# Kernel tuning notes

Measured on AMD Instinct MI355X. Metric: run time of the kernel, lower is better.

Reference implementation:

```python
import jax, jax.numpy as jnp
import numpy as np

HEADS = 4
DIM_HEAD = 32


def setup_inputs() -> dict:
    key = jax.random.key(0)
    k0, k1, k2, k3 = jax.random.split(key, 4)
    b, C, H, W = 32, 128, 64, 64
    hidden = HEADS * DIM_HEAD
    x = jax.random.normal(k0, (b, C, H, W), dtype=jnp.float32)
    g = jnp.ones((C,), dtype=jnp.float32)                      # RMSNorm gain
    w_qkv = jax.random.normal(k1, (3 * hidden, C), dtype=jnp.float32) * 0.05
    mem_kv = jax.random.normal(k2, (2, HEADS, DIM_HEAD, 4), dtype=jnp.float32)
    w_out = jax.random.normal(k3, (C, hidden), dtype=jnp.float32) * 0.05
    b_out = jnp.zeros((C,), dtype=jnp.float32)
    return {"x": x, "g": g, "w_qkv": w_qkv, "mem_kv": mem_kv,
            "w_out": w_out, "b_out": b_out}


def reference(x, g, w_qkv, mem_kv, w_out, b_out):
    b, C, H, W = x.shape
    heads = mem_kv.shape[1]
    dh = mem_kv.shape[2]
    hidden = heads * dh
    scale = dh ** -0.5

    # RMSNorm variant: F.normalize along channel dim * g * sqrt(C)
    norm = jnp.maximum(jnp.sqrt(jnp.sum(x * x, axis=1, keepdims=True)), 1e-12)
    xn = x / norm * g[None, :, None, None] * (C ** 0.5)

    # 1x1 conv qkv projection (no bias)
    qkv = jnp.einsum('bchw,oc->bohw', xn, w_qkv)  # [b, 3*hidden, H, W]
    q, k, v = jnp.split(qkv, 3, axis=1)
    n = H * W
    q = q.reshape(b, heads, dh, n)
    k = k.reshape(b, heads, dh, n)
    v = v.reshape(b, heads, dh, n)

    # prepend memory kv slots along the token dim
    mk = jnp.broadcast_to(mem_kv[0][None], (b, heads, dh, mem_kv.shape[3]))
    mv = jnp.broadcast_to(mem_kv[1][None], (b, heads, dh, mem_kv.shape[3]))
    k = jnp.concatenate([mk, k], axis=-1)
    v = jnp.concatenate([mv, v], axis=-1)

    q = jax.nn.softmax(q, axis=-2) * scale   # softmax over feature dim d
    k = jax.nn.softmax(k, axis=-1)           # softmax over token dim n

    context = jnp.einsum('bhdn,bhen->bhde', k, v)   # [b,h,d,e]
    out = jnp.einsum('bhde,bhdn->bhen', context, q)  # [b,h,e,n]
    out = out.reshape(b, hidden, H, W)

    # 1x1 conv output projection (with bias)
    return jnp.einsum('bchw,oc->bohw', out, w_out) + b_out[None, :, None, None]
```

## Files before the change

kernel.cpp:

```cpp
#include <hip/hip_runtime.h>
#include <hip/hip_bf16.h>

typedef __attribute__((ext_vector_type(8))) short short8;
typedef __attribute__((ext_vector_type(4))) short bf16x4;
typedef __attribute__((ext_vector_type(4))) float f32x4;


__device__ __forceinline__ unsigned short f2bf(float f) {
  unsigned u = __float_as_uint(f);
  u += 0x7fff + ((u >> 16) & 1);
  return (unsigned short)(u >> 16);
}
__device__ __forceinline__ float bf2f(unsigned short s) {
  return __uint_as_float(((unsigned)s) << 16);
}

__global__ void k0_init(const float* __restrict__ wqkv, const float* __restrict__ g,
                        float* __restrict__ ws) {
  int tid = blockIdx.x * blockDim.x + threadIdx.x;
  int stride = gridDim.x * blockDim.x;
  unsigned short* Wf = (unsigned short*)(ws + 2424832);
  for (int i = tid; i < 49152; i += stride) {
    int o = i >> 7, c = i & 127;
    int f = (o >> 4) * 4 + (c >> 5);
    int lane = (o & 15) + (((c >> 3) & 3) << 4);
    Wf[f * 512 + lane * 8 + (c & 7)] = f2bf(wqkv[o * 128 + c]);
  }
  float* gs = ws + 2449408;
  if (tid < 128) gs[tid] = g[tid] * 11.313708498984761f;
}

__global__ __launch_bounds__(256, 2) void k1_qkv(
    const float* __restrict__ x, const unsigned short* __restrict__ Wf,
    const float* __restrict__ gs, unsigned short* __restrict__ Sp,
    unsigned short* __restrict__ Zp, unsigned short* __restrict__ qbf) {
  __shared__ __align__(16) unsigned short xnf[16 * 512];
  __shared__ __align__(16) unsigned short kbuf[128 * 64];
  __shared__ __align__(16) unsigned short vbuf[128 * 64];
  __shared__ float ssred[256];
  const int b = blockIdx.x >> 4, grp = blockIdx.x & 15;
  const int tid = threadIdx.x;
  const int p = tid & 63, w = tid >> 6;
  const int chunk = __builtin_amdgcn_readfirstlane(w);
  const int l = p, quad = l >> 4, l16 = l & 15;

  short8 ones;
#pragma unroll
  for (int j = 0; j < 8; j++) ones[j] = (short)0x3F80;

  f32x4 accS[2][2] = {};
  f32x4 accZ[2] = {};

  const float* xbase = x + (size_t)b * 524288;
  float xr[32];
  {
    const float* xb = xbase + grp * 256 + p;
#pragma unroll
    for (int i = 0; i < 32; i++) xr[i] = xb[(size_t)(chunk * 32 + i) * 4096];
  }

#pragma unroll 1
  for (int t = 0; t < 4; t++) {
    const int tile = grp * 4 + t;
    float ss = 0.f;
#pragma unroll
    for (int i = 0; i < 32; i++) ss += xr[i] * xr[i];
    ssred[w * 64 + p] = ss;
    __syncthreads();
    float tot = ssred[p] + ssred[64 + p] + ssred[128 + p] + ssred[192 + p];
    float inv = 1.0f / fmaxf(sqrtf(tot), 1e-12f);
#pragma unroll
    for (int q8 = 0; q8 < 4; q8++) {
      short8 v8;
#pragma unroll
      for (int j = 0; j < 8; j++) {
        int i = q8 * 8 + j;
        v8[j] = (short)f2bf(xr[i] * gs[chunk * 32 + i] * inv);
      }
      *(short8*)&xnf[(chunk * 4 + (p >> 4)) * 512 + ((p & 15) + q8 * 16) * 8] = v8;
    }
    __syncthreads();

    if (t < 3) {
      const float* xb = xbase + (tile + 1) * 64 + p;
#pragma unroll
      for (int i = 0; i < 32; i++) xr[i] = xb[(size_t)(chunk * 32 + i) * 4096];
    }

    const short8* Wfv = (const short8*)Wf;
#pragma unroll
    for (int s = 0; s < 3; s++) {
      f32x4 acc[2][4] = {};
#pragma unroll
      for (int k0 = 0; k0 < 4; k0++) {
        short8 bfr[4];
#pragma unroll
        for (int n0 = 0; n0 < 4; n0++)
          bfr[n0] = *(const short8*)&xnf[(k0 * 4 + n0) * 512 + l * 8];
#pragma unroll
        for (int off = 0; off < 2; off++) {
          short8 afr = Wfv[((s * 8 + chunk * 2 + off) * 4 + k0) * 64 + l];
#pragma unroll
          for (int n0 = 0; n0 < 4; n0++)
            acc[off][n0] = __builtin_amdgcn_mfma_f32_16x16x32_bf16(afr, bfr[n0], acc[off][n0], 0, 0, 0);
        }
      }
      if (s == 0) {
#pragma unroll
        for (int n0 = 0; n0 < 4; n0++) {
          float m = -1e30f;
#pragma unroll
          for (int off = 0; off < 2; off++)
#pragma unroll
            for (int r = 0; r < 4; r++) m = fmaxf(m, acc[off][n0][r]);
          m = fmaxf(m, __shfl_xor(m, 16, 64));
          m = fmaxf(m, __shfl_xor(m, 32, 64));
          float e[2][4]; float sum = 0.f;
#pragma unroll
          for (int off = 0; off < 2; off++)
#pragma unroll
            for (int r = 0; r < 4; r++) {
              e[off][r] = __expf(acc[off][n0][r] - m);
              sum += e[off][r];
            }
          sum += __shfl_xor(sum, 16, 64);
          sum += __shfl_xor(sum, 32, 64);
          float rs = 0.17677669529663687f / sum;
          int qbase = ((b * 64 + tile) * 16 + chunk * 4 + n0) * 512;
#pragma unroll
          for (int off = 0; off < 2; off++) {
            int lane2 = l16 + ((off * 2 + (quad >> 1)) << 4);
            bf16x4 qv;
#pragma unroll
            for (int r = 0; r < 4; r++) qv[r] = (short)f2bf(e[off][r] * rs);
            *(bf16x4*)&qbf[qbase + lane2 * 8 + (quad & 1) * 4] = qv;
          }
        }
      } else if (s == 1) {
#pragma unroll
        for (int off = 0; off < 2; off++)
#pragma unroll
          for (int n0 = 0; n0 < 4; n0++)
#pragma unroll
            for (int r = 0; r < 4; r++) {
              int row = off * 16 + quad * 4 + r;
              int px = n0 * 16 + l16;
              kbuf[(chunk * 32 + row) * 64 + (px ^ ((row & 7) << 3))] = f2bf(__expf(acc[off][n0][r]));
            }
      } else {
#pragma unroll
        for (int off = 0; off < 2; off++)
#pragma unroll
          for (int n0 = 0; n0 < 4; n0++)
#pragma unroll
            for (int r = 0; r < 4; r++) {
              int row = off * 16 + quad * 4 + r;
              int px = n0 * 16 + l16;
              vbuf[(chunk * 32 + row) * 64 + (px ^ ((row & 7) << 3))] = f2bf(acc[off][n0][r]);
            }
      }
    }

    const unsigned short* kb = kbuf + chunk * 2048;
    const unsigned short* vb = vbuf + chunk * 2048;
#pragma unroll
    for (int kk = 0; kk < 2; kk++) {
      int cofs = (kk * 32 + quad * 8) ^ ((l16 & 7) << 3);
      short8 ak[2], av[2];
#pragma unroll
      for (int mm = 0; mm < 2; mm++) {
        ak[mm] = *(const short8*)&kb[(mm * 16 + l16) * 64 + cofs];
        av[mm] = *(const short8*)&vb[(mm * 16 + l16) * 64 + cofs];
      }
#pragma unroll
      for (int mm = 0; mm < 2; mm++) {
#pragma unroll
        for (int nn = 0; nn < 2; nn++)
          accS[mm][nn] = __builtin_amdgcn_mfma_f32_16x16x32_bf16(ak[mm], av[nn], accS[mm][nn], 0, 0, 0);
        accZ[mm] = __builtin_amdgcn_mfma_f32_16x16x32_bf16(ak[mm], ones, accZ[mm], 0, 0, 0);
      }
    }
  }

  unsigned short* Spb = Sp + (size_t)(b * 16 + grp) * 4096 + chunk * 1024;
#pragma unroll
  for (int mm = 0; mm < 2; mm++)
#pragma unroll
    for (int nn = 0; nn < 2; nn++) {
      bf16x4 sv;
#pragma unroll
      for (int r = 0; r < 4; r++) sv[r] = (short)f2bf(accS[mm][nn][r]);
      *(bf16x4*)&Spb[(mm * 2 + nn) * 256 + l * 4] = sv;
    }
  if (l16 == 0) {
#pragma unroll
    for (int mm = 0; mm < 2; mm++) {
      bf16x4 zv;
#pragma unroll
      for (int r = 0; r < 4; r++) zv[r] = (short)f2bf(accZ[mm][r]);
      *(bf16x4*)&Zp[(b * 16 + grp) * 128 + chunk * 32 + mm * 16 + quad * 4] = zv;
    }
  }
}

__global__ __launch_bounds__(256) void k2_ctx(
    const unsigned short* __restrict__ Sp, const unsigned short* __restrict__ Zp,
    const float* __restrict__ memkv, const float* __restrict__ wout,
    unsigned short* __restrict__ Mtf) {
  __shared__ float wl[128 * 33];
  __shared__ float Cs[8 * 32];
  __shared__ float zsh[8];
  __shared__ float zinv_s[8];
  const int b = blockIdx.x >> 4, sl = blockIdx.x & 15, tid = threadIdx.x;
  const int hd0 = sl * 8, h = hd0 >> 5;
  for (int i = tid; i < 4096; i += 256) {
    int o = i >> 5, e = i & 31;
    wl[o * 33 + e] = wout[o * 128 + h * 32 + e];
  }
  {
    int hdi = tid >> 5, g = tid & 31;
    float zp = (g < 16) ? bf2f(Zp[(b * 16 + g) * 128 + hd0 + hdi]) : 0.f;
#pragma unroll
    for (int s2 = 1; s2 < 32; s2 <<= 1) zp += __shfl_xor(zp, s2, 32);
    if (g == 0) zsh[hdi] = zp;
  }
  __syncthreads();
  if (tid < 8) {
    int hd = hd0 + tid;
    float zm = 0.f;
#pragma unroll
    for (int j = 0; j < 4; j++) zm += __expf(memkv[hd * 4 + j]);
    zinv_s[tid] = 1.0f / (zsh[tid] + zm);
  }
  __syncthreads();
  {
    int hdi = tid >> 5, e = tid & 31;
    int hd = hd0 + hdi, d = hd & 31;
    int fofs = h * 1024 + ((d >> 4) * 2 + (e >> 4)) * 256 + ((e & 15) + ((d >> 2) & 3) * 16) * 4 + (d & 3);
    const unsigned short* Spb = Sp + (size_t)b * 65536 + fofs;
    float s = 0.f;
#pragma unroll
    for (int g = 0; g < 16; g++) s += bf2f(Spb[g * 4096]);
    float sm = 0.f;
#pragma unroll
    for (int j = 0; j < 4; j++)
      sm += __expf(memkv[hd * 4 + j]) * memkv[512 + (h * 32 + e) * 4 + j];
    Cs[hdi * 32 + e] = (s + sm) * zinv_s[hdi];
  }
  __syncthreads();
  for (int i = tid; i < 1024; i += 256) {
    int o = i & 127, hdi = i >> 7;
    float a = 0.f;
#pragma unroll
    for (int e = 0; e < 32; e++) a += wl[o * 33 + e] * Cs[hdi * 32 + e];
    int hd = hd0 + hdi;
    int f = (o >> 4) * 4 + h;
    int lane = (o & 15) + (((hd >> 3) & 3) << 4);
    Mtf[(size_t)b * 16384 + f * 512 + lane * 8 + (hd & 7)] = f2bf(a);
  }
}

__global__ __launch_bounds__(256) void k3_out(
    const unsigned short* __restrict__ qbf, const unsigned short* __restrict__ Mtf,
    const float* __restrict__ bout, float* __restrict__ out) {
  const int b = blockIdx.x >> 6, tile = blockIdx.x & 63;
  const int tid = threadIdx.x;
  const int l = tid & 63, quad = l >> 4, l16 = l & 15;
  const int chunk = __builtin_amdgcn_readfirstlane(tid >> 6);
  const short8* Mv = (const short8*)Mtf;
  const short8* qv = (const short8*)qbf + (size_t)(b * 64 + tile) * 1024;
  short8 afr[2][4];
#pragma unroll
  for (int mm = 0; mm < 2; mm++)
#pragma unroll
    for (int k0 = 0; k0 < 4; k0++)
      afr[mm][k0] = Mv[((size_t)b * 32 + (chunk * 2 + mm) * 4 + k0) * 64 + l];
  f32x4 acc[2][4] = {};
#pragma unroll
  for (int hh = 0; hh < 2; hh++) {
    short8 bfr[8];
#pragma unroll
    for (int j = 0; j < 8; j++) bfr[j] = qv[(hh * 8 + j) * 64 + l];
#pragma unroll
    for (int kk = 0; kk < 2; kk++) {
      int k0 = hh * 2 + kk;
#pragma unroll
      for (int mm = 0; mm < 2; mm++)
#pragma unroll
        for (int n0 = 0; n0 < 4; n0++)
          acc[mm][n0] = __builtin_amdgcn_mfma_f32_16x16x32_bf16(afr[mm][k0], bfr[kk * 4 + n0], acc[mm][n0], 0, 0, 0);
    }
  }
  float* ob = out + (size_t)b * 524288 + tile * 64;
#pragma unroll
  for (int mm = 0; mm < 2; mm++)
#pragma unroll
    for (int r = 0; r < 4; r++) {
      int o = chunk * 32 + mm * 16 + quad * 4 + r;
      float bv = bout[o];
#pragma unroll
      for (int n0 = 0; n0 < 4; n0++)
        ob[(size_t)o * 4096 + n0 * 16 + l16] = acc[mm][n0][r] + bv;
    }
}

extern "C" void kernel_launch(void* const* d_in, const int* in_sizes, int n_in,
                              void* d_out, int out_size, void* d_ws, size_t ws_size,
                              hipStream_t stream) {
  const float* x     = (const float*)d_in[0];
  const float* g     = (const float*)d_in[1];
  const float* wqkv  = (const float*)d_in[2];
  const float* memkv = (const float*)d_in[3];
  const float* wout  = (const float*)d_in[4];
  const float* bout  = (const float*)d_in[5];
  float* out = (float*)d_out;
  float* ws = (float*)d_ws;
  unsigned short* Sp  = (unsigned short*)ws;
  unsigned short* Zp  = (unsigned short*)(ws + 2097152);
  unsigned short* Mtf = (unsigned short*)(ws + 2162688);
  unsigned short* Wf  = (unsigned short*)(ws + 2424832);
  float* gs  = ws + 2449408;
  unsigned short* qbf = (unsigned short*)(ws + 2449536);

  k0_init<<<128, 256, 0, stream>>>(wqkv, g, ws);
  k1_qkv<<<512, 256, 0, stream>>>(x, Wf, gs, Sp, Zp, qbf);
  k2_ctx<<<512, 256, 0, stream>>>(Sp, Zp, memkv, wout, Mtf);
  k3_out<<<2048, 256, 0, stream>>>(qbf, Mtf, bout, out);
}
```

Before: 187.5 us.

## Fuse four kernels into one persistent kernel with global atomic barriers

Merges the weight-prep, QKV/context-partial, context-reduce and output-projection kernels into a single 512-block kernel. Grid-wide atomic spin barriers separate the phases, and the counters are zeroed by a memset before launch. This removes three kernel launch gaps and tail effects. In exchange it needs all 512 blocks co-resident (2 per CU via launch bounds) to avoid deadlock, and the k3 phase now runs 4 tiles per block instead of 2048 separate blocks.

```diff
diff --git a/kernel.cpp b/kernel.cpp
--- a/kernel.cpp
+++ b/kernel.cpp
@@ -15,293 +15,315 @@
   return __uint_as_float(((unsigned)s) << 16);
 }
 
-__global__ void k0_init(const float* __restrict__ wqkv, const float* __restrict__ g,
-                        float* __restrict__ ws) {
-  int tid = blockIdx.x * blockDim.x + threadIdx.x;
-  int stride = gridDim.x * blockDim.x;
-  unsigned short* Wf = (unsigned short*)(ws + 2424832);
-  for (int i = tid; i < 49152; i += stride) {
-    int o = i >> 7, c = i & 127;
-    int f = (o >> 4) * 4 + (c >> 5);
-    int lane = (o & 15) + (((c >> 3) & 3) << 4);
-    Wf[f * 512 + lane * 8 + (c & 7)] = f2bf(wqkv[o * 128 + c]);
-  }
-  float* gs = ws + 2449408;
-  if (tid < 128) gs[tid] = g[tid] * 11.313708498984761f;
-}
-
-__global__ __launch_bounds__(256, 2) void k1_qkv(
-    const float* __restrict__ x, const unsigned short* __restrict__ Wf,
-    const float* __restrict__ gs, unsigned short* __restrict__ Sp,
-    unsigned short* __restrict__ Zp, unsigned short* __restrict__ qbf) {
-  __shared__ __align__(16) unsigned short xnf[16 * 512];
-  __shared__ __align__(16) unsigned short kbuf[128 * 64];
-  __shared__ __align__(16) unsigned short vbuf[128 * 64];
-  __shared__ float ssred[256];
-  const int b = blockIdx.x >> 4, grp = blockIdx.x & 15;
+__device__ __forceinline__ void gbar(unsigned* c, unsigned nb) {
+  __threadfence();
+  __syncthreads();
+  if (threadIdx.x == 0) {
+    atomicAdd(c, 1u);
+    while (__hip_atomic_load(c, __ATOMIC_RELAXED, __HIP_MEMORY_SCOPE_AGENT) < nb)
+      __builtin_amdgcn_s_sleep(2);
+  }
+  __syncthreads();
+  __threadfence();
+}
+
+__global__ __launch_bounds__(256, 2) void fused(
+    const float* __restrict__ x, const float* __restrict__ gvec,
+    const float* __restrict__ wqkv, const float* __restrict__ memkv,
+    const float* __restrict__ wout, const float* __restrict__ bout,
+    float* __restrict__ out, float* __restrict__ ws) {
+  __shared__ __align__(16) unsigned char smem[50176];
+
+  const int bid = blockIdx.x;
+  const int b = bid >> 4, grp = bid & 15;
   const int tid = threadIdx.x;
   const int p = tid & 63, w = tid >> 6;
   const int chunk = __builtin_amdgcn_readfirstlane(w);
   const int l = p, quad = l >> 4, l16 = l & 15;
 
-  short8 ones;
-#pragma unroll
-  for (int j = 0; j < 8; j++) ones[j] = (short)0x3F80;
-
-  f32x4 accS[2][2] = {};
-  f32x4 accZ[2] = {};
-
-  const float* xbase = x + (size_t)b * 524288;
-  float xr[32];
+  unsigned short* Sp  = (unsigned short*)ws;
+  unsigned short* Zp  = (unsigned short*)(ws + 2097152);
+  unsigned*       cnt = (unsigned*)(ws + 2129920);
+  unsigned short* Mtf = (unsigned short*)(ws + 2162688);
+  unsigned short* Wf  = (unsigned short*)(ws + 2424832);
+  float* gs           = ws + 2449408;
+  unsigned short* qbf = (unsigned short*)(ws + 2449536);
+
   {
-    const float* xb = xbase + grp * 256 + p;
-#pragma unroll
-    for (int i = 0; i < 32; i++) xr[i] = xb[(size_t)(chunk * 32 + i) * 4096];
-  }
+    int gtid = bid * 256 + tid;
+    if (gtid < 49152) {
+      int o = gtid >> 7, c = gtid & 127;
+      int f = (o >> 4) * 4 + (c >> 5);
+      int lane = (o & 15) + (((c >> 3) & 3) << 4);
+      Wf[f * 512 + lane * 8 + (c & 7)] = f2bf(wqkv[o * 128 + c]);
+    }
+    if (gtid < 128) gs[gtid] = gvec[gtid] * 11.313708498984761f;
+  }
+  gbar(cnt + 0, 512);
+
+  {
+    unsigned short* xnf  = (unsigned short*)smem;
+    unsigned short* kbuf = (unsigned short*)(smem + 16384);
+    unsigned short* vbuf = (unsigned short*)(smem + 32768);
+    float* ssred         = (float*)(smem + 49152);
+
+    short8 ones;
+#pragma unroll
+    for (int j = 0; j < 8; j++) ones[j] = (short)0x3F80;
+
+    f32x4 accS[2][2] = {};
+    f32x4 accZ[2] = {};
+
+    const float* xbase = x + (size_t)b * 524288;
+    float xr[32];
+    {
+      const float* xb = xbase + grp * 256 + p;
+#pragma unroll
+      for (int i = 0; i < 32; i++) xr[i] = xb[(size_t)(chunk * 32 + i) * 4096];
+    }
 
 #pragma unroll 1
-  for (int t = 0; t < 4; t++) {
-    const int tile = grp * 4 + t;
-    float ss = 0.f;
-#pragma unroll
-    for (int i = 0; i < 32; i++) ss += xr[i] * xr[i];
-    ssred[w * 64 + p] = ss;
+    for (int t = 0; t < 4; t++) {
+      const int tile = grp * 4 + t;
+      float ss = 0.f;
+#pragma unroll
+      for (int i = 0; i < 32; i++) ss += xr[i] * xr[i];
+      ssred[w * 64 + p] = ss;
+      __syncthreads();
+      float tot = ssred[p] + ssred[64 + p] + ssred[128 + p] + ssred[192 + p];
+      float inv = 1.0f / fmaxf(sqrtf(tot), 1e-12f);
+#pragma unroll
+      for (int q8 = 0; q8 < 4; q8++) {
+        short8 v8;
+#pragma unroll
+        for (int j = 0; j < 8; j++) {
+          int i = q8 * 8 + j;
+          v8[j] = (short)f2bf(xr[i] * gs[chunk * 32 + i] * inv);
+        }
+        *(short8*)&xnf[(chunk * 4 + (p >> 4)) * 512 + ((p & 15) + q8 * 16) * 8] = v8;
+      }
+      __syncthreads();
+
+      if (t < 3) {
+        const float* xb = xbase + (tile + 1) * 64 + p;
+#pragma unroll
+        for (int i = 0; i < 32; i++) xr[i] = xb[(size_t)(chunk * 32 + i) * 4096];
+      }
+
+      const short8* Wfv = (const short8*)Wf;
+#pragma unroll
+      for (int s = 0; s < 3; s++) {
+        f32x4 acc[2][4] = {};
+#pragma unroll
+        for (int k0 = 0; k0 < 4; k0++) {
+          short8 bfr[4];
+#pragma unroll
+          for (int n0 = 0; n0 < 4; n0++)
+            bfr[n0] = *(const short8*)&xnf[(k0 * 4 + n0) * 512 + l * 8];
+#pragma unroll
+          for (int off = 0; off < 2; off++) {
+            short8 afr = Wfv[((s * 8 + chunk * 2 + off) * 4 + k0) * 64 + l];
+#pragma unroll
+            for (int n0 = 0; n0 < 4; n0++)
+              acc[off][n0] = __builtin_amdgcn_mfma_f32_16x16x32_bf16(afr, bfr[n0], acc[off][n0], 0, 0, 0);
+          }
+        }
+        if (s == 0) {
+#pragma unroll
+          for (int n0 = 0; n0 < 4; n0++) {
+            float m = -1e30f;
+#pragma unroll
+            for (int off = 0; off < 2; off++)
+#pragma unroll
+              for (int r = 0; r < 4; r++) m = fmaxf(m, acc[off][n0][r]);
+            m = fmaxf(m, __shfl_xor(m, 16, 64));
+            m = fmaxf(m, __shfl_xor(m, 32, 64));
+            float e[2][4]; float sum = 0.f;
+#pragma unroll
+            for (int off = 0; off < 2; off++)
+#pragma unroll
+              for (int r = 0; r < 4; r++) {
+                e[off][r] = __expf(acc[off][n0][r] - m);
+                sum += e[off][r];
+              }
+            sum += __shfl_xor(sum, 16, 64);
+            sum += __shfl_xor(sum, 32, 64);
+            float rs = 0.17677669529663687f / sum;
+            int qbase = ((b * 64 + tile) * 16 + chunk * 4 + n0) * 512;
+#pragma unroll
+            for (int off = 0; off < 2; off++) {
+              int lane2 = l16 + ((off * 2 + (quad >> 1)) << 4);
+              bf16x4 qv;
+#pragma unroll
+              for (int r = 0; r < 4; r++) qv[r] = (short)f2bf(e[off][r] * rs);
+              *(bf16x4*)&qbf[qbase + lane2 * 8 + (quad & 1) * 4] = qv;
+            }
+          }
+        } else if (s == 1) {
+#pragma unroll
+          for (int off = 0; off < 2; off++)
+#pragma unroll
+            for (int n0 = 0; n0 < 4; n0++)
+#pragma unroll
+              for (int r = 0; r < 4; r++) {
+                int row = off * 16 + quad * 4 + r;
+                int px = n0 * 16 + l16;
+                kbuf[(chunk * 32 + row) * 64 + (px ^ ((row & 7) << 3))] = f2bf(__expf(acc[off][n0][r]));
+              }
+        } else {
+#pragma unroll
+          for (int off = 0; off < 2; off++)
+#pragma unroll
+            for (int n0 = 0; n0 < 4; n0++)
+#pragma unroll
+              for (int r = 0; r < 4; r++) {
+                int row = off * 16 + quad * 4 + r;
+                int px = n0 * 16 + l16;
+                vbuf[(chunk * 32 + row) * 64 + (px ^ ((row & 7) << 3))] = f2bf(acc[off][n0][r]);
+              }
+        }
+      }
+
+      const unsigned short* kb = kbuf + chunk * 2048;
+      const unsigned short* vb = vbuf + chunk * 2048;
+#pragma unroll
+      for (int kk = 0; kk < 2; kk++) {
+        int cofs = (kk * 32 + quad * 8) ^ ((l16 & 7) << 3);
+        short8 ak[2], av[2];
+#pragma unroll
+        for (int mm = 0; mm < 2; mm++) {
+          ak[mm] = *(const short8*)&kb[(mm * 16 + l16) * 64 + cofs];
+          av[mm] = *(const short8*)&vb[(mm * 16 + l16) * 64 + cofs];
+        }
+#pragma unroll
+        for (int mm = 0; mm < 2; mm++) {
+#pragma unroll
+          for (int nn = 0; nn < 2; nn++)
+            accS[mm][nn] = __builtin_amdgcn_mfma_f32_16x16x32_bf16(ak[mm], av[nn], accS[mm][nn], 0, 0, 0);
+          accZ[mm] = __builtin_amdgcn_mfma_f32_16x16x32_bf16(ak[mm], ones, accZ[mm], 0, 0, 0);
+        }
+      }
+    }
+
+    unsigned short* Spb = Sp + (size_t)(b * 16 + grp) * 4096 + chunk * 1024;
+#pragma unroll
+    for (int mm = 0; mm < 2; mm++)
+#pragma unroll
+      for (int nn = 0; nn < 2; nn++) {
+        bf16x4 sv;
+#pragma unroll
+        for (int r = 0; r < 4; r++) sv[r] = (short)f2bf(accS[mm][nn][r]);
+        *(bf16x4*)&Spb[(mm * 2 + nn) * 256 + l * 4] = sv;
+      }
+    if (l16 == 0) {
+#pragma unroll
+      for (int mm = 0; mm < 2; mm++) {
+        bf16x4 zv;
+#pragma unroll
+        for (int r = 0; r < 4; r++) zv[r] = (short)f2bf(accZ[mm][r]);
+        *(bf16x4*)&Zp[(b * 16 + grp) * 128 + chunk * 32 + mm * 16 + quad * 4] = zv;
+      }
+    }
+  }
+  gbar(cnt + 1, 512);
+
+  {
+    float* wl     = (float*)smem;
+    float* Cs     = (float*)(smem + 16896);
+    float* zsh    = (float*)(smem + 17920);
+    float* zinv_s = (float*)(smem + 17952);
+    const int sl = grp;
+    const int hd0 = sl * 8, h = hd0 >> 5;
+    for (int i = tid; i < 4096; i += 256) {
+      int o = i >> 5, e = i & 31;
+      wl[o * 33 + e] = wout[o * 128 + h * 32 + e];
+    }
+    {
+      int hdi = tid >> 5, g = tid & 31;
+      float zp = (g < 16) ? bf2f(Zp[(b * 16 + g) * 128 + hd0 + hdi]) : 0.f;
+#pragma unroll
+      for (int s2 = 1; s2 < 32; s2 <<= 1) zp += __shfl_xor(zp, s2, 32);
+      if (g == 0) zsh[hdi] = zp;
+    }
     __syncthreads();
-    float tot = ssred[p] + ssred[64 + p] + ssred[128 + p] + ssred[192 + p];
-    float inv = 1.0f / fmaxf(sqrtf(tot), 1e-12f);
-#pragma unroll
-    for (int q8 = 0; q8 < 4; q8++) {
-      short8 v8;
-#pragma unroll
-      for (int j = 0; j < 8; j++) {
-        int i = q8 * 8 + j;
-        v8[j] = (short)f2bf(xr[i] * gs[chunk * 32 + i] * inv);
-      }
-      *(short8*)&xnf[(chunk * 4 + (p >> 4)) * 512 + ((p & 15) + q8 * 16) * 8] = v8;
+    if (tid < 8) {
+      int hd = hd0 + tid;
+      float zm = 0.f;
+#pragma unroll
+      for (int j = 0; j < 4; j++) zm += __expf(memkv[hd * 4 + j]);
+      zinv_s[tid] = 1.0f / (zsh[tid] + zm);
     }
     __syncthreads();
-
-    if (t < 3) {
-      const float* xb = xbase + (tile + 1) * 64 + p;
-#pragma unroll
-      for (int i = 0; i < 32; i++) xr[i] = xb[(size_t)(chunk * 32 + i) * 4096];
-    }
-
-    const short8* Wfv = (const short8*)Wf;
-#pragma unroll
-    for (int s = 0; s < 3; s++) {
+    {
+      int hdi = tid >> 5, e = tid & 31;
+      int hd = hd0 + hdi, d = hd & 31;
+      int fofs = h * 1024 + ((d >> 4) * 2 + (e >> 4)) * 256 + ((e & 15) + ((d >> 2) & 3) * 16) * 4 + (d & 3);
+      const unsigned short* Spb = Sp + (size_t)b * 65536 + fofs;
+      float s = 0.f;
+#pragma unroll
+      for (int g = 0; g < 16; g++) s += bf2f(Spb[g * 4096]);
+      float sm = 0.f;
+#pragma unroll
+      for (int j = 0; j < 4; j++)
+        sm += __expf(memkv[hd * 4 + j]) * memkv[512 + (h * 32 + e) * 4 + j];
+      Cs[hdi * 32 + e] = (s + sm) * zinv_s[hdi];
+    }
+    __syncthreads();
+    for (int i = tid; i < 1024; i += 256) {
+      int o = i & 127, hdi = i >> 7;
+      float a = 0.f;
+#pragma unroll
+      for (int e = 0; e < 32; e++) a += wl[o * 33 + e] * Cs[hdi * 32 + e];
+      int hd = hd0 + hdi;
+      int f = (o >> 4) * 4 + h;
+      int lane = (o & 15) + (((hd >> 3) & 3) << 4);
+      Mtf[(size_t)b * 16384 + f * 512 + lane * 8 + (hd & 7)] = f2bf(a);
+    }
+  }
+  gbar(cnt + 2, 512);
+
+  {
+    const short8* Mv = (const short8*)Mtf;
+    short8 afr[2][4];
+#pragma unroll
+    for (int mm = 0; mm < 2; mm++)
+#pragma unroll
+      for (int k0 = 0; k0 < 4; k0++)
+        afr[mm][k0] = Mv[((size_t)b * 32 + (chunk * 2 + mm) * 4 + k0) * 64 + l];
+    float* obb = out + (size_t)b * 524288;
+#pragma unroll 1
+    for (int t = 0; t < 4; t++) {
+      const int tile = grp * 4 + t;
+      const short8* qv = (const short8*)qbf + (size_t)(b * 64 + tile) * 1024;
       f32x4 acc[2][4] = {};
 #pragma unroll
-      for (int k0 = 0; k0 < 4; k0++) {
-        short8 bfr[4];
-#pragma unroll
-        for (int n0 = 0; n0 < 4; n0++)
-          bfr[n0] = *(const short8*)&xnf[(k0 * 4 + n0) * 512 + l * 8];
-#pragma unroll
-        for (int off = 0; off < 2; off++) {
-          short8 afr = Wfv[((s * 8 + chunk * 2 + off) * 4 + k0) * 64 + l];
+      for (int hh = 0; hh < 2; hh++) {
+        short8 bfr[8];
+#pragma unroll
+        for (int j = 0; j < 8; j++) bfr[j] = qv[(hh * 8 + j) * 64 + l];
+#pragma unroll
+        for (int kk = 0; kk < 2; kk++) {
+          int k0 = hh * 2 + kk;
+#pragma unroll
+          for (int mm = 0; mm < 2; mm++)
+#pragma unroll
+            for (int n0 = 0; n0 < 4; n0++)
+              acc[mm][n0] = __builtin_amdgcn_mfma_f32_16x16x32_bf16(afr[mm][k0], bfr[kk * 4 + n0], acc[mm][n0], 0, 0, 0);
+        }
+      }
+      float* ob = obb + tile * 64;
+#pragma unroll
+      for (int mm = 0; mm < 2; mm++)
+#pragma unroll
+        for (int r = 0; r < 4; r++) {
+          int o = chunk * 32 + mm * 16 + quad * 4 + r;
+          float bv = bout[o];
 #pragma unroll
           for (int n0 = 0; n0 < 4; n0++)
-            acc[off][n0] = __builtin_amdgcn_mfma_f32_16x16x32_bf16(afr, bfr[n0], acc[off][n0], 0, 0, 0);
-        }
-      }
-      if (s == 0) {
-#pragma unroll
-        for (int n0 = 0; n0 < 4; n0++) {
-          float m = -1e30f;
-#pragma unroll
-          for (int off = 0; off < 2; off++)
-#pragma unroll
-            for (int r = 0; r < 4; r++) m = fmaxf(m, acc[off][n0][r]);
-          m = fmaxf(m, __shfl_xor(m, 16, 64));
-          m = fmaxf(m, __shfl_xor(m, 32, 64));
-          float e[2][4]; float sum = 0.f;
-#pragma unroll
-          for (int off = 0; off < 2; off++)
-#pragma unroll
-            for (int r = 0; r < 4; r++) {
-              e[off][r] = __expf(acc[off][n0][r] - m);
-              sum += e[off][r];
-            }
-          sum += __shfl_xor(sum, 16, 64);
-          sum += __shfl_xor(sum, 32, 64);
-          float rs = 0.17677669529663687f / sum;
-          int qbase = ((b * 64 + tile) * 16 + chunk * 4 + n0) * 512;
-#pragma unroll
-          for (int off = 0; off < 2; off++) {
-            int lane2 = l16 + ((off * 2 + (quad >> 1)) << 4);
-            bf16x4 qv;
-#pragma unroll
-            for (int r = 0; r < 4; r++) qv[r] = (short)f2bf(e[off][r] * rs);
-            *(bf16x4*)&qbf[qbase + lane2 * 8 + (quad & 1) * 4] = qv;
-          }
-        }
-      } else if (s == 1) {
-#pragma unroll
-        for (int off = 0; off < 2; off++)
-#pragma unroll
-          for (int n0 = 0; n0 < 4; n0++)
-#pragma unroll
-            for (int r = 0; r < 4; r++) {
-              int row = off * 16 + quad * 4 + r;
-              int px = n0 * 16 + l16;
-              kbuf[(chunk * 32 + row) * 64 + (px ^ ((row & 7) << 3))] = f2bf(__expf(acc[off][n0][r]));
-            }
-      } else {
-#pragma unroll
-        for (int off = 0; off < 2; off++)
-#pragma unroll
-          for (int n0 = 0; n0 < 4; n0++)
-#pragma unroll
-            for (int r = 0; r < 4; r++) {
-              int row = off * 16 + quad * 4 + r;
-              int px = n0 * 16 + l16;
-              vbuf[(chunk * 32 + row) * 64 + (px ^ ((row & 7) << 3))] = f2bf(acc[off][n0][r]);
-            }
-      }
-    }
-
-    const unsigned short* kb = kbuf + chunk * 2048;
-    const unsigned short* vb = vbuf + chunk * 2048;
-#pragma unroll
-    for (int kk = 0; kk < 2; kk++) {
-      int cofs = (kk * 32 + quad * 8) ^ ((l16 & 7) << 3);
-      short8 ak[2], av[2];
-#pragma unroll
-      for (int mm = 0; mm < 2; mm++) {
-        ak[mm] = *(const short8*)&kb[(mm * 16 + l16) * 64 + cofs];
-        av[mm] = *(const short8*)&vb[(mm * 16 + l16) * 64 + cofs];
-      }
-#pragma unroll
-      for (int mm = 0; mm < 2; mm++) {
-#pragma unroll
-        for (int nn = 0; nn < 2; nn++)
-          accS[mm][nn] = __builtin_amdgcn_mfma_f32_16x16x32_bf16(ak[mm], av[nn], accS[mm][nn], 0, 0, 0);
-        accZ[mm] = __builtin_amdgcn_mfma_f32_16x16x32_bf16(ak[mm], ones, accZ[mm], 0, 0, 0);
-      }
-    }
-  }
-
-  unsigned short* Spb = Sp + (size_t)(b * 16 + grp) * 4096 + chunk * 1024;
-#pragma unroll
-  for (int mm = 0; mm < 2; mm++)
-#pragma unroll
-    for (int nn = 0; nn < 2; nn++) {
-      bf16x4 sv;
-#pragma unroll
-      for (int r = 0; r < 4; r++) sv[r] = (short)f2bf(accS[mm][nn][r]);
-      *(bf16x4*)&Spb[(mm * 2 + nn) * 256 + l * 4] = sv;
-    }
-  if (l16 == 0) {
-#pragma unroll
-    for (int mm = 0; mm < 2; mm++) {
-      bf16x4 zv;
-#pragma unroll
-      for (int r = 0; r < 4; r++) zv[r] = (short)f2bf(accZ[mm][r]);
-      *(bf16x4*)&Zp[(b * 16 + grp) * 128 + chunk * 32 + mm * 16 + quad * 4] = zv;
-    }
-  }
-}
-
-__global__ __launch_bounds__(256) void k2_ctx(
-    const unsigned short* __restrict__ Sp, const unsigned short* __restrict__ Zp,
-    const float* __restrict__ memkv, const float* __restrict__ wout,
-    unsigned short* __restrict__ Mtf) {
-  __shared__ float wl[128 * 33];
-  __shared__ float Cs[8 * 32];
-  __shared__ float zsh[8];
-  __shared__ float zinv_s[8];
-  const int b = blockIdx.x >> 4, sl = blockIdx.x & 15, tid = threadIdx.x;
-  const int hd0 = sl * 8, h = hd0 >> 5;
-  for (int i = tid; i < 4096; i += 256) {
-    int o = i >> 5, e = i & 31;
-    wl[o * 33 + e] = wout[o * 128 + h * 32 + e];
-  }
-  {
-    int hdi = tid >> 5, g = tid & 31;
-    float zp = (g < 16) ? bf2f(Zp[(b * 16 + g) * 128 + hd0 + hdi]) : 0.f;
-#pragma unroll
-    for (int s2 = 1; s2 < 32; s2 <<= 1) zp += __shfl_xor(zp, s2, 32);
-    if (g == 0) zsh[hdi] = zp;
-  }
-  __syncthreads();
-  if (tid < 8) {
-    int hd = hd0 + tid;
-    float zm = 0.f;
-#pragma unroll
-    for (int j = 0; j < 4; j++) zm += __expf(memkv[hd * 4 + j]);
-    zinv_s[tid] = 1.0f / (zsh[tid] + zm);
-  }
-  __syncthreads();
-  {
-    int hdi = tid >> 5, e = tid & 31;
-    int hd = hd0 + hdi, d = hd & 31;
-    int fofs = h * 1024 + ((d >> 4) * 2 + (e >> 4)) * 256 + ((e & 15) + ((d >> 2) & 3) * 16) * 4 + (d & 3);
-    const unsigned short* Spb = Sp + (size_t)b * 65536 + fofs;
-    float s = 0.f;
-#pragma unroll
-    for (int g = 0; g < 16; g++) s += bf2f(Spb[g * 4096]);
-    float sm = 0.f;
-#pragma unroll
-    for (int j = 0; j < 4; j++)
-      sm += __expf(memkv[hd * 4 + j]) * memkv[512 + (h * 32 + e) * 4 + j];
-    Cs[hdi * 32 + e] = (s + sm) * zinv_s[hdi];
-  }
-  __syncthreads();
-  for (int i = tid; i < 1024; i += 256) {
-    int o = i & 127, hdi = i >> 7;
-    float a = 0.f;
-#pragma unroll
-    for (int e = 0; e < 32; e++) a += wl[o * 33 + e] * Cs[hdi * 32 + e];
-    int hd = hd0 + hdi;
-    int f = (o >> 4) * 4 + h;
-    int lane = (o & 15) + (((hd >> 3) & 3) << 4);
-    Mtf[(size_t)b * 16384 + f * 512 + lane * 8 + (hd & 7)] = f2bf(a);
-  }
-}
-
-__global__ __launch_bounds__(256) void k3_out(
-    const unsigned short* __restrict__ qbf, const unsigned short* __restrict__ Mtf,
-    const float* __restrict__ bout, float* __restrict__ out) {
-  const int b = blockIdx.x >> 6, tile = blockIdx.x & 63;
-  const int tid = threadIdx.x;
-  const int l = tid & 63, quad = l >> 4, l16 = l & 15;
-  const int chunk = __builtin_amdgcn_readfirstlane(tid >> 6);
-  const short8* Mv = (const short8*)Mtf;
-  const short8* qv = (const short8*)qbf + (size_t)(b * 64 + tile) * 1024;
-  short8 afr[2][4];
-#pragma unroll
-  for (int mm = 0; mm < 2; mm++)
-#pragma unroll
-    for (int k0 = 0; k0 < 4; k0++)
-      afr[mm][k0] = Mv[((size_t)b * 32 + (chunk * 2 + mm) * 4 + k0) * 64 + l];
-  f32x4 acc[2][4] = {};
-#pragma unroll
-  for (int hh = 0; hh < 2; hh++) {
-    short8 bfr[8];
-#pragma unroll
-    for (int j = 0; j < 8; j++) bfr[j] = qv[(hh * 8 + j) * 64 + l];
-#pragma unroll
-    for (int kk = 0; kk < 2; kk++) {
-      int k0 = hh * 2 + kk;
-#pragma unroll
-      for (int mm = 0; mm < 2; mm++)
-#pragma unroll
-        for (int n0 = 0; n0 < 4; n0++)
-          acc[mm][n0] = __builtin_amdgcn_mfma_f32_16x16x32_bf16(afr[mm][k0], bfr[kk * 4 + n0], acc[mm][n0], 0, 0, 0);
-    }
-  }
-  float* ob = out + (size_t)b * 524288 + tile * 64;
-#pragma unroll
-  for (int mm = 0; mm < 2; mm++)
-#pragma unroll
-    for (int r = 0; r < 4; r++) {
-      int o = chunk * 32 + mm * 16 + quad * 4 + r;
-      float bv = bout[o];
-#pragma unroll
-      for (int n0 = 0; n0 < 4; n0++)
-        ob[(size_t)o * 4096 + n0 * 16 + l16] = acc[mm][n0][r] + bv;
-    }
+            ob[(size_t)o * 4096 + n0 * 16 + l16] = acc[mm][n0][r] + bv;
+        }
+    }
+  }
 }
 
 extern "C" void kernel_launch(void* const* d_in, const int* in_sizes, int n_in,
@@ -315,15 +337,7 @@
   const float* bout  = (const float*)d_in[5];
   float* out = (float*)d_out;
   float* ws = (float*)d_ws;
-  unsigned short* Sp  = (unsigned short*)ws;
-  unsigned short* Zp  = (unsigned short*)(ws + 2097152);
-  unsigned short* Mtf = (unsigned short*)(ws + 2162688);
-  unsigned short* Wf  = (unsigned short*)(ws + 2424832);
-  float* gs  = ws + 2449408;
-  unsigned short* qbf = (unsigned short*)(ws + 2449536);
-
-  k0_init<<<128, 256, 0, stream>>>(wqkv, g, ws);
-  k1_qkv<<<512, 256, 0, stream>>>(x, Wf, gs, Sp, Zp, qbf);
-  k2_ctx<<<512, 256, 0, stream>>>(Sp, Zp, memkv, wout, Mtf);
-  k3_out<<<2048, 256, 0, stream>>>(qbf, Mtf, bout, out);
-}
+
+  hipMemsetAsync((char*)d_ws + 8519680, 0, 16, stream);
+  fused<<<512, 256, 0, stream>>>(x, g, wqkv, memkv, wout, bout, out, ws);
+}
```

Result: slower. 446.2 us (+137.9%).
